# Kernel optimization log

Hardware: AMD Instinct MI355X
Metric: run time of the kernel (lower is better)

## Reference

```python
import jax, jax.numpy as jnp
import numpy as np

B, D, E, H, O, K = 8192, 3072, 8, 2048, 512, 2
EPS = float(np.finfo(float).eps)  # np.finfo(float).eps used in SparseDispatcher.combine


def _cv_squared(v):
    # torch .var() is unbiased (ddof=1)
    v = v.astype(jnp.float32)
    return jnp.var(v, ddof=1) / (jnp.mean(v) ** 2 + 1e-10)


def setup_inputs() -> dict:
    key = jax.random.key(0)
    ks = jax.random.split(key, 8)
    x = jax.random.normal(ks[0], (B, D), dtype=jnp.float32)
    Cats = jax.random.uniform(ks[1], (B, E), dtype=jnp.float32)
    w_gate = jax.random.normal(ks[2], (D, E), dtype=jnp.float32) * 0.01
    # per-expert 2-layer MLP standing in for the per-expert ResNet
    W1 = jax.random.normal(ks[3], (E, D, H), dtype=jnp.float32) * (1.0 / np.sqrt(D))
    b1 = jnp.zeros((E, H), dtype=jnp.float32)
    W2 = jax.random.normal(ks[4], (E, H, O), dtype=jnp.float32) * (1.0 / np.sqrt(H))
    b2 = jnp.zeros((E, O), dtype=jnp.float32)
    return {"x": x, "Cats": Cats, "w_gate": w_gate, "W1": W1, "b1": b1,
            "W2": W2, "b2": b2, "train": 0}


def reference(x, Cats, w_gate, W1, b1, W2, b2, train):
    # ---- top_k_gating (eval path; train branch mutates optimizer state) ----
    logits = x @ w_gate                                   # [B, E]
    top_vals, top_idx = jax.lax.top_k(logits, min(K + 1, E))
    top_k_vals = top_vals[:, :K]                          # [B, K]
    top_k_idx = top_idx[:, :K]                            # [B, K]
    top_k_gates = jax.nn.softmax(top_k_vals, axis=1)      # softmax over kept logits
    rows = jnp.arange(x.shape[0])[:, None]
    gates = jnp.zeros_like(logits).at[rows, top_k_idx].set(top_k_gates)  # scatter

    load = (gates > 0).sum(axis=0)                        # tokens per expert
    importance = gates.sum(axis=0)
    aux_loss = 0.01 * (_cv_squared(importance) + _cv_squared(load))

    # ---- dispatch / expert / combine ----
    # Dense grouped form: expert_i runs on its routed tokens; tokens with
    # gates[b,i]==0 contribute exactly 0 to the combine, identical math to
    # SparseDispatcher's gather/split + exp*gate + index_add + log.
    h = jax.nn.relu(jnp.einsum('bd,edh->beh', x, W1) + b1[None])  # [B, E, H]
    out = jnp.einsum('beh,eho->beo', h, W2) + b2[None]            # [B, E, O]
    combined = jnp.einsum('be,beo->bo', gates, jnp.exp(out))      # exp, *gate, sum
    combined = jnp.where(combined == 0, EPS, combined)
    y = jnp.log(combined)
    return (y, aux_loss)
```

## Files before the change

### kernel.cpp

```cpp
#include <hip/hip_runtime.h>
#include <stdint.h>


typedef __bf16 bf16x8 __attribute__((ext_vector_type(8)));
typedef __bf16 bf16x4 __attribute__((ext_vector_type(4)));
typedef float floatx4 __attribute__((ext_vector_type(4)));

#define EPSF 2.2204460492503131e-16f

__device__ __forceinline__ void gl_lds16(const void* g, void* l) {
  __builtin_amdgcn_global_load_lds(
      (__attribute__((address_space(1))) void*)(g),
      (__attribute__((address_space(3))) void*)(l), 16, 0, 0);
}

__global__ __launch_bounds__(512) void k_gating(
    const float* __restrict__ x, const float* __restrict__ wg,
    __bf16* __restrict__ x_bf, int* __restrict__ expsel,
    float* __restrict__ gpair) {
  __shared__ float wgs[12320];
  const int tid = threadIdx.x;
  const int lane = tid & 63;
  const int w = tid >> 6;
  const int r = blockIdx.x * 8 + w;
  const int g = lane >> 3;
  const int e = lane & 7;
  const float* xr = x + (size_t)r * 3072;
  __bf16* xbr = x_bf + (size_t)r * 3072;

#pragma unroll
  for (int t = 0; t < 12; ++t) {
    const int d = t * 256 + lane * 4;
    const float4 xv = *(const float4*)(xr + d);
    bf16x4 xo;
    xo.x = (__bf16)xv.x; xo.y = (__bf16)xv.y;
    xo.z = (__bf16)xv.z; xo.w = (__bf16)xv.w;
    *(bf16x4*)(xbr + d) = xo;
  }

  double a0 = 0.0, a1 = 0.0;
  for (int h = 0; h < 2; ++h) {
    __syncthreads();
#pragma unroll
    for (int t = 0; t < 6; ++t) {
      const int wi = t * 2048 + tid * 4;
      const int gg = wi / 1536;
      const float4 v = *(const float4*)(wg + h * 12288 + wi);
      *(float4*)(wgs + wi + 4 * gg) = v;
    }
    __syncthreads();
    const float* xrg = xr + h * 1536 + g * 192;
    const float* wbase = wgs + g * 1540 + e;
    for (int i = 0; i < 192; i += 4) {
      const float4 xv = *(const float4*)(xrg + i);
      a0 += (double)xv.x * (double)wbase[(i + 0) * 8];
      a1 += (double)xv.y * (double)wbase[(i + 1) * 8];
      a0 += (double)xv.z * (double)wbase[(i + 2) * 8];
      a1 += (double)xv.w * (double)wbase[(i + 3) * 8];
    }
  }
  double v = a0 + a1;
  v += __shfl_xor(v, 8);
  v += __shfl_xor(v, 16);
  v += __shfl_xor(v, 32);
  double le[8];
#pragma unroll
  for (int ee = 0; ee < 8; ++ee) le[ee] = __shfl(v, ee);
  if (lane == 0) {
    int i0 = 0; double v0 = le[0];
#pragma unroll
    for (int k = 1; k < 8; ++k) if (le[k] > v0) { v0 = le[k]; i0 = k; }
    int i1 = (i0 == 0) ? 1 : 0; double v1 = le[i1];
#pragma unroll
    for (int k = 0; k < 8; ++k)
      if (k != i0 && le[k] > v1 && k != i1) { v1 = le[k]; i1 = k; }
    const float tt = (float)exp(v1 - v0);
    const float g0 = 1.0f / (1.0f + tt);
    const float g1 = tt / (1.0f + tt);
    expsel[r] = i0 | (i1 << 4);
    gpair[r * 2] = g0;
    gpair[r * 2 + 1] = g1;
  }
}

__global__ __launch_bounds__(256) void k_build_lists(
    const int* __restrict__ expsel, const float* __restrict__ gpair,
    int* __restrict__ lists, int* __restrict__ cnt, double* __restrict__ imp) {
  const int e = blockIdx.x;
  const int tid = threadIdx.x;
  const int lane = tid & 63;
  const int w = tid >> 6;
  __shared__ int wsum[4];
  __shared__ double dsum[4];
  int base = 0;
  double gsum = 0.0;
  int* out = lists + e * 8192;
  for (int c = 0; c < 32; ++c) {
    const int r = c * 256 + tid;
    const int sel = expsel[r];
    const bool m0 = ((sel & 15) == e);
    const bool m1 = (((sel >> 4) & 15) == e);
    const bool m = m0 || m1;
    const int entry = 2 * r + (m1 ? 1 : 0);
    const unsigned long long mask = __ballot(m);
    const int wcount = __popcll(mask);
    const int pos = __popcll(mask & ((1ull << lane) - 1ull));
    if (lane == 0) wsum[w] = wcount;
    __syncthreads();
    int pre = base;
#pragma unroll
    for (int ww = 0; ww < 4; ++ww) if (ww < w) pre += wsum[ww];
    const int total = wsum[0] + wsum[1] + wsum[2] + wsum[3];
    if (m) {
      out[pre + pos] = entry;
      gsum += (double)gpair[entry];
    }
    base += total;
    __syncthreads();
  }
  gsum += __shfl_down(gsum, 32);
  gsum += __shfl_down(gsum, 16);
  gsum += __shfl_down(gsum, 8);
  gsum += __shfl_down(gsum, 4);
  gsum += __shfl_down(gsum, 2);
  gsum += __shfl_down(gsum, 1);
  if (lane == 0) dsum[w] = gsum;
  __syncthreads();
  if (tid == 0) {
    imp[e] = dsum[0] + dsum[1] + dsum[2] + dsum[3];
    cnt[e] = base;
  }
}

__global__ void k_sched_aux(const int* __restrict__ cnt, const double* __restrict__ imp,
                            int* __restrict__ sched, int* __restrict__ nslots,
                            float* __restrict__ aux_out) {
  if (threadIdx.x != 0 || blockIdx.x != 0) return;
  int ns = 0;
  for (int e = 0; e < 8; ++e) {
    const int c = cnt[e];
    const int t = (c + 127) >> 7;
    for (int i = 0; i < t; ++i) { sched[2 * ns] = e; sched[2 * ns + 1] = i << 7; ++ns; }
  }
  *nslots = ns;
  double mi = 0.0, ml = 0.0;
  for (int e = 0; e < 8; ++e) { mi += imp[e]; ml += (double)cnt[e]; }
  mi *= 0.125; ml *= 0.125;
  double vi = 0.0, vl = 0.0;
  for (int e = 0; e < 8; ++e) {
    const double di = imp[e] - mi; vi += di * di;
    const double dl = (double)cnt[e] - ml; vl += dl * dl;
  }
  vi /= 7.0; vl /= 7.0;
  aux_out[0] = (float)(0.01 * (vi / (mi * mi + 1e-10) + vl / (ml * ml + 1e-10)));
}

__global__ __launch_bounds__(256) void k_transpose_cvt(
    const float* __restrict__ in, __bf16* __restrict__ out, int R, int C) {
  __shared__ float tile[64][65];
  const int e = blockIdx.z;
  const int c0 = blockIdx.x * 64;
  const int r0 = blockIdx.y * 64;
  const float* src = in + (size_t)e * R * C + (size_t)r0 * C + c0;
  __bf16* dst = out + (size_t)e * R * C + (size_t)c0 * R + r0;
  const int tx = threadIdx.x & 15;
  const int ty = threadIdx.x >> 4;
#pragma unroll
  for (int i = 0; i < 4; ++i) {
    const int row = ty + i * 16;
    const float4 v = *(const float4*)(src + (size_t)row * C + tx * 4);
    tile[row][tx * 4 + 0] = v.x;
    tile[row][tx * 4 + 1] = v.y;
    tile[row][tx * 4 + 2] = v.z;
    tile[row][tx * 4 + 3] = v.w;
  }
  __syncthreads();
#pragma unroll
  for (int i = 0; i < 4; ++i) {
    const int cc = ty + i * 16;
    const int rr = tx * 4;
    bf16x4 o;
    o.x = (__bf16)tile[rr + 0][cc];
    o.y = (__bf16)tile[rr + 1][cc];
    o.z = (__bf16)tile[rr + 2][cc];
    o.w = (__bf16)tile[rr + 3][cc];
    *(bf16x4*)(dst + (size_t)cc * R + rr) = o;
  }
}

template <int KDIM, int MODE>
__global__ __launch_bounds__(256, 2) void k_moe_gemm(
    const __bf16* __restrict__ Asrc, const __bf16* __restrict__ Ball,
    const float* __restrict__ bias, const int* __restrict__ lists,
    const int* __restrict__ cnt, const int* __restrict__ sched,
    const int* __restrict__ nslots, const float* __restrict__ gpair,
    __bf16* __restrict__ hout, float* __restrict__ oout) {
  constexpr int NDIM = (MODE == 0) ? 2048 : 512;
  const int slot = blockIdx.y;
  if (slot >= *nslots) return;
  const int e = sched[2 * slot];
  const int row0 = sched[2 * slot + 1];
  const int cnte = cnt[e];
  const int n0 = blockIdx.x * 128;

  __shared__ unsigned short As[128 * 32];
  __shared__ unsigned short Bs[128 * 32];

  const int tid = threadIdx.x;
  const int lane = tid & 63;
  const int wid = __builtin_amdgcn_readfirstlane(tid >> 6);
  const int wm = wid >> 1;
  const int wn = wid & 1;

  const __bf16* Be = Ball + (size_t)e * NDIM * KDIM;
  const int* liste = lists + e * 8192;
  const int acol = (lane & 3) * 8;

  const __bf16* aptr[2];
  const __bf16* bptr[2];
#pragma unroll
  for (int p = 0; p < 2; ++p) {
    const int chunk = wid + 4 * p;
    const int lr = chunk * 16 + (lane >> 2);
    int m = row0 + lr;
    m = (m < cnte) ? m : (cnte - 1);
    const int entry = liste[m];
    const int srow = (MODE == 0) ? (entry >> 1) : entry;
    aptr[p] = Asrc + (size_t)srow * KDIM + acol;
    bptr[p] = Be + (size_t)(n0 + lr) * KDIM + acol;
  }

  floatx4 acc[4][4];
#pragma unroll
  for (int i = 0; i < 4; ++i)
#pragma unroll
    for (int j = 0; j < 4; ++j) {
      acc[i][j].x = 0.f; acc[i][j].y = 0.f; acc[i][j].z = 0.f; acc[i][j].w = 0.f;
    }

  for (int k0 = 0; k0 < KDIM; k0 += 32) {
#pragma unroll
    for (int p = 0; p < 2; ++p) {
      gl_lds16(aptr[p] + k0, &As[(wid + 4 * p) * 512]);
      gl_lds16(bptr[p] + k0, &Bs[(wid + 4 * p) * 512]);
    }
    __syncthreads();
    bf16x8 af[4], bfr[4];
    const int rdoff = (lane & 15) * 32 + (lane >> 4) * 8;
#pragma unroll
    for (int i = 0; i < 4; ++i)
      af[i] = *(const bf16x8*)&As[(wm * 64 + i * 16) * 32 + rdoff];
#pragma unroll
    for (int j = 0; j < 4; ++j)
      bfr[j] = *(const bf16x8*)&Bs[(wn * 64 + j * 16) * 32 + rdoff];
    __syncthreads();
#pragma unroll
    for (int i = 0; i < 4; ++i)
#pragma unroll
      for (int j = 0; j < 4; ++j)
        acc[i][j] = __builtin_amdgcn_mfma_f32_16x16x32_bf16(af[i], bfr[j], acc[i][j], 0, 0, 0);
  }

  const int cq = lane >> 4;
  const int cn = lane & 15;
#pragma unroll
  for (int i = 0; i < 4; ++i) {
#pragma unroll
    for (int r = 0; r < 4; ++r) {
      const int m = row0 + wm * 64 + i * 16 + cq * 4 + r;
      if (m < cnte) {
        const int p = liste[m];
        if (MODE == 0) {
          __bf16* orow = hout + (size_t)p * 2048;
#pragma unroll
          for (int j = 0; j < 4; ++j) {
            const int n = n0 + wn * 64 + j * 16 + cn;
            float v = acc[i][j][r] + bias[e * 2048 + n];
            v = v > 0.0f ? v : 0.0f;
            orow[n] = (__bf16)v;
          }
        } else {
          float* orow = oout + (size_t)p * 512;
          const float g = gpair[p];
#pragma unroll
          for (int j = 0; j < 4; ++j) {
            const int n = n0 + wn * 64 + j * 16 + cn;
            const float v = acc[i][j][r] + bias[e * 512 + n];
            orow[n] = g * __expf(v);
          }
        }
      }
    }
  }
}

__global__ __launch_bounds__(128) void k_combine(const float* __restrict__ op,
                                                 float* __restrict__ y) {
  const int r = blockIdx.x;
  const int o = threadIdx.x * 4;
  const float4 a = *(const float4*)(op + (size_t)(2 * r) * 512 + o);
  const float4 b = *(const float4*)(op + (size_t)(2 * r + 1) * 512 + o);
  float4 res;
  float s;
  s = a.x + b.x; if (s == 0.0f) s = EPSF; res.x = logf(s);
  s = a.y + b.y; if (s == 0.0f) s = EPSF; res.y = logf(s);
  s = a.z + b.z; if (s == 0.0f) s = EPSF; res.z = logf(s);
  s = a.w + b.w; if (s == 0.0f) s = EPSF; res.w = logf(s);
  *(float4*)(y + (size_t)r * 512 + o) = res;
}

extern "C" void kernel_launch(void* const* d_in, const int* in_sizes, int n_in,
                              void* d_out, int out_size, void* d_ws, size_t ws_size,
                              hipStream_t stream) {
  (void)in_sizes; (void)n_in; (void)out_size; (void)ws_size;
  const float* x  = (const float*)d_in[0];
  const float* wg = (const float*)d_in[2];
  const float* W1 = (const float*)d_in[3];
  const float* b1 = (const float*)d_in[4];
  const float* W2 = (const float*)d_in[5];
  const float* b2 = (const float*)d_in[6];
  float* y = (float*)d_out;

  char* w = (char*)d_ws;
  __bf16* x_bf = (__bf16*)w; w += (size_t)8192 * 3072 * 2;
  __bf16* w1t  = (__bf16*)w; w += (size_t)8 * 2048 * 3072 * 2;
  __bf16* w2t  = (__bf16*)w; w += (size_t)8 * 512 * 2048 * 2;
  __bf16* hp   = (__bf16*)w; w += (size_t)16384 * 2048 * 2;
  float*  op   = (float*)w;  w += (size_t)16384 * 512 * 4;
  int*    lists= (int*)w;    w += (size_t)8 * 8192 * 4;
  float*  gpr  = (float*)w;  w += (size_t)16384 * 4;
  int*    expsel=(int*)w;    w += (size_t)8192 * 4;
  int*    cnt  = (int*)w;    w += 64;
  double* imp  = (double*)w; w += 64;
  int*    sched= (int*)w;    w += 2 * 136 * 4;
  int*    nslots=(int*)w;    w += 64;

  hipLaunchKernelGGL(k_gating, dim3(1024), dim3(512), 0, stream, x, wg, x_bf, expsel, gpr);
  hipLaunchKernelGGL(k_build_lists, dim3(8), dim3(256), 0, stream, expsel, gpr, lists, cnt, imp);
  hipLaunchKernelGGL(k_transpose_cvt, dim3(32, 48, 8), dim3(256), 0, stream, W1, w1t, 3072, 2048);
  hipLaunchKernelGGL(k_transpose_cvt, dim3(8, 32, 8), dim3(256), 0, stream, W2, w2t, 2048, 512);
  hipLaunchKernelGGL(k_sched_aux, dim3(1), dim3(64), 0, stream, cnt, imp, sched, nslots,
                     y + (size_t)8192 * 512);
  hipLaunchKernelGGL((k_moe_gemm<3072, 0>), dim3(16, 136), dim3(256), 0, stream,
                     x_bf, w1t, b1, lists, cnt, sched, nslots, (const float*)nullptr,
                     hp, (float*)nullptr);
  hipLaunchKernelGGL((k_moe_gemm<2048, 1>), dim3(4, 136), dim3(256), 0, stream,
                     hp, w2t, b2, lists, cnt, sched, nslots, gpr,
                     (__bf16*)nullptr, op);
  hipLaunchKernelGGL(k_combine, dim3(8192), dim3(128), 0, stream, op, y);
}
```

Baseline: 803.5 us.

## Add 256-row-tile first expert GEMM with XCD-aware block remap and swizzled LDS

```diff
diff --git a/kernel.cpp b/kernel.cpp
--- a/kernel.cpp
+++ b/kernel.cpp
@@ -134,15 +134,19 @@
 
 __global__ void k_sched_aux(const int* __restrict__ cnt, const double* __restrict__ imp,
                             int* __restrict__ sched, int* __restrict__ nslots,
+                            int* __restrict__ sched2, int* __restrict__ nslots2,
                             float* __restrict__ aux_out) {
   if (threadIdx.x != 0 || blockIdx.x != 0) return;
-  int ns = 0;
+  int ns = 0, ns2 = 0;
   for (int e = 0; e < 8; ++e) {
     const int c = cnt[e];
     const int t = (c + 127) >> 7;
     for (int i = 0; i < t; ++i) { sched[2 * ns] = e; sched[2 * ns + 1] = i << 7; ++ns; }
+    const int t2 = (c + 255) >> 8;
+    for (int i = 0; i < t2; ++i) { sched2[2 * ns2] = e; sched2[2 * ns2 + 1] = i << 8; ++ns2; }
   }
   *nslots = ns;
+  *nslots2 = ns2;
   double mi = 0.0, ml = 0.0;
   for (int e = 0; e < 8; ++e) { mi += imp[e]; ml += (double)cnt[e]; }
   mi *= 0.125; ml *= 0.125;
@@ -185,6 +189,126 @@
     o.z = (__bf16)tile[rr + 2][cc];
     o.w = (__bf16)tile[rr + 3][cc];
     *(bf16x4*)(dst + (size_t)cc * R + rr) = o;
+  }
+}
+
+template <int KDIM>
+__global__ __launch_bounds__(512, 2) void k_moe_gemm256(
+    const __bf16* __restrict__ Asrc, const __bf16* __restrict__ Ball,
+    const float* __restrict__ bias, const int* __restrict__ lists,
+    const int* __restrict__ cnt, const int* __restrict__ sched,
+    const int* __restrict__ nslots, __bf16* __restrict__ hout) {
+  constexpr int NT = KDIM / 64;
+  __shared__ __bf16 lds2[2 * 24576];
+
+  const int nwg = gridDim.x * gridDim.y;
+  int lin = blockIdx.y * gridDim.x + blockIdx.x;
+  const int q = nwg >> 3, r = nwg & 7;
+  const int xcd = lin & 7, idx = lin >> 3;
+  lin = (xcd < r) ? (xcd * (q + 1) + idx) : (r * (q + 1) + (xcd - r) * q + idx);
+  const int slot = lin >> 4;
+  const int ntile = lin & 15;
+  if (slot >= *nslots) return;
+
+  const int e = sched[2 * slot];
+  const int row0 = sched[2 * slot + 1];
+  const int cnte = cnt[e];
+  if (cnte <= 0) return;
+  const int n0 = ntile * 128;
+
+  const int tid = threadIdx.x;
+  const int lane = tid & 63;
+  const int w = __builtin_amdgcn_readfirstlane(tid >> 6);
+  const int wm = w >> 1;
+  const int wn = w & 1;
+  const int lr = lane >> 3;
+  const int kc = (lane & 7) ^ lr;
+
+  const __bf16* Be = Ball + (size_t)e * 2048 * KDIM;
+  const int* liste = lists + e * 8192;
+
+  const __bf16* aptr[4];
+#pragma unroll
+  for (int j = 0; j < 4; ++j) {
+    int m = row0 + w * 32 + j * 8 + lr;
+    m = (m < cnte) ? m : (cnte - 1);
+    aptr[j] = Asrc + (size_t)(liste[m] >> 1) * KDIM + kc * 8;
+  }
+  const __bf16* bptr[2];
+#pragma unroll
+  for (int j = 0; j < 2; ++j)
+    bptr[j] = Be + (size_t)(n0 + w * 16 + j * 8 + lr) * KDIM + kc * 8;
+
+  floatx4 acc[4][4];
+#pragma unroll
+  for (int i = 0; i < 4; ++i)
+#pragma unroll
+    for (int j = 0; j < 4; ++j) {
+      acc[i][j].x = 0.f; acc[i][j].y = 0.f; acc[i][j].z = 0.f; acc[i][j].w = 0.f;
+    }
+
+  auto STAGE = [&](int buf, int kt) {
+    __bf16* base = lds2 + buf * 24576;
+    const int ko = kt * 64;
+#pragma unroll
+    for (int j = 0; j < 4; ++j)
+      gl_lds16(aptr[j] + ko, base + (w * 32 + j * 8) * 64);
+#pragma unroll
+    for (int j = 0; j < 2; ++j)
+      gl_lds16(bptr[j] + ko, base + 16384 + (w * 16 + j * 8) * 64);
+  };
+
+  STAGE(0, 0);
+
+  const int frow = lane & 15;
+  const int fr7 = lane & 7;
+  const int fch = lane >> 4;
+  const int axo0 = ((fch) ^ fr7) * 8;
+  const int axo1 = ((4 + fch) ^ fr7) * 8;
+
+  for (int kt = 0; kt < NT; ++kt) {
+    __syncthreads();
+    if (kt + 1 < NT) STAGE((kt + 1) & 1, kt + 1);
+    const __bf16* Abuf = lds2 + (kt & 1) * 24576;
+    const __bf16* Bbuf = Abuf + 16384;
+    bf16x8 bfr[2][4];
+#pragma unroll
+    for (int j = 0; j < 4; ++j) {
+      const __bf16* brow = Bbuf + (wn * 64 + j * 16 + frow) * 64;
+      bfr[0][j] = *(const bf16x8*)(brow + axo0);
+      bfr[1][j] = *(const bf16x8*)(brow + axo1);
+    }
+#pragma unroll
+    for (int i = 0; i < 4; ++i) {
+      const __bf16* arow = Abuf + (wm * 64 + i * 16 + frow) * 64;
+      const bf16x8 a0 = *(const bf16x8*)(arow + axo0);
+      const bf16x8 a1 = *(const bf16x8*)(arow + axo1);
+#pragma unroll
+      for (int j = 0; j < 4; ++j) {
+        acc[i][j] = __builtin_amdgcn_mfma_f32_16x16x32_bf16(a0, bfr[0][j], acc[i][j], 0, 0, 0);
+        acc[i][j] = __builtin_amdgcn_mfma_f32_16x16x32_bf16(a1, bfr[1][j], acc[i][j], 0, 0, 0);
+      }
+    }
+  }
+
+  const int cq = lane >> 4;
+  const int cn = lane & 15;
+#pragma unroll
+  for (int i = 0; i < 4; ++i) {
+#pragma unroll
+    for (int rr = 0; rr < 4; ++rr) {
+      const int m = row0 + wm * 64 + i * 16 + cq * 4 + rr;
+      if (m < cnte) {
+        const int p = liste[m];
+        __bf16* orow = hout + (size_t)p * 2048;
+#pragma unroll
+        for (int j = 0; j < 4; ++j) {
+          const int n = n0 + wn * 64 + j * 16 + cn;
+          float v = acc[i][j][rr] + bias[e * 2048 + n];
+          orow[n] = (__bf16)(v > 0.0f ? v : 0.0f);
+        }
+      }
+    }
   }
 }
 
@@ -201,6 +325,7 @@
   const int e = sched[2 * slot];
   const int row0 = sched[2 * slot + 1];
   const int cnte = cnt[e];
+  if (cnte <= 0) return;
   const int n0 = blockIdx.x * 128;
 
   __shared__ unsigned short As[128 * 32];
@@ -334,16 +459,17 @@
   double* imp  = (double*)w; w += 64;
   int*    sched= (int*)w;    w += 2 * 136 * 4;
   int*    nslots=(int*)w;    w += 64;
+  int*    sched2=(int*)w;    w += 2 * 72 * 4;
+  int*    nslots2=(int*)w;   w += 64;
 
   hipLaunchKernelGGL(k_gating, dim3(1024), dim3(512), 0, stream, x, wg, x_bf, expsel, gpr);
   hipLaunchKernelGGL(k_build_lists, dim3(8), dim3(256), 0, stream, expsel, gpr, lists, cnt, imp);
   hipLaunchKernelGGL(k_transpose_cvt, dim3(32, 48, 8), dim3(256), 0, stream, W1, w1t, 3072, 2048);
   hipLaunchKernelGGL(k_transpose_cvt, dim3(8, 32, 8), dim3(256), 0, stream, W2, w2t, 2048, 512);
   hipLaunchKernelGGL(k_sched_aux, dim3(1), dim3(64), 0, stream, cnt, imp, sched, nslots,
-                     y + (size_t)8192 * 512);
-  hipLaunchKernelGGL((k_moe_gemm<3072, 0>), dim3(16, 136), dim3(256), 0, stream,
-                     x_bf, w1t, b1, lists, cnt, sched, nslots, (const float*)nullptr,
-                     hp, (float*)nullptr);
+                     sched2, nslots2, y + (size_t)8192 * 512);
+  hipLaunchKernelGGL((k_moe_gemm256<3072>), dim3(16, 72), dim3(512), 0, stream,
+                     x_bf, w1t, b1, lists, cnt, sched2, nslots2, hp);
   hipLaunchKernelGGL((k_moe_gemm<2048, 1>), dim3(4, 136), dim3(256), 0, stream,
                      hp, w2t, b2, lists, cnt, sched, nslots, gpr,
                      (__bf16*)nullptr, op);
```

Result: no change. 808.8 us (+0.7%).
